# Kernel tuning notes

Hardware: AMD Instinct MI355X
Metric: run time of the kernel (lower is better)

Reference implementation:

```python
import jax, jax.numpy as jnp
import numpy as np

E = 8        # numExperts
D = 1024     # d_model
F = 4096     # expert hidden = 4*d_model
T = 8192     # total tokens (sum of expertFrequency)


def setup_inputs() -> dict:
    key = jax.random.key(0)
    k0, k1, k2, k3, k4 = jax.random.split(key, 5)
    expertOrderedInput = jax.random.normal(k0, (T, D), dtype=jnp.float32)
    # Static equal split so the split sizes are jit-compatible.
    expertFrequency = jnp.full((E,), T // E, dtype=jnp.int64)
    s1 = 1.0 / np.sqrt(D)
    s2 = 1.0 / np.sqrt(F)
    w1 = jax.random.normal(k1, (E, D, F), dtype=jnp.float32) * s1
    b1 = jnp.zeros((E, F), dtype=jnp.float32)
    w2 = jax.random.normal(k2, (E, F, D), dtype=jnp.float32) * s2
    b2 = jnp.zeros((E, D), dtype=jnp.float32)
    return {"expertOrderedInput": expertOrderedInput,
            "expertFrequency": expertFrequency,
            "w1": w1, "b1": b1, "w2": w2, "b2": b2}


def reference(expertOrderedInput, expertFrequency, w1, b1, w2, b2):
    # expertOrderedInput: [T, D], tokens pre-sorted by expert.
    # expertFrequency is equal per expert (T/E each), so the
    # split-loop-cat in the torch module is exactly a grouped GEMM.
    e = w1.shape[0]
    t = expertOrderedInput.shape[0]
    x = expertOrderedInput.reshape(e, t // e, -1)            # [E, T/E, D]
    h = jax.nn.gelu(jnp.einsum('etd,edf->etf', x, w1) + b1[:, None, :])
    y = jnp.einsum('etf,efd->etd', h, w2) + b2[:, None, :]   # [E, T/E, D]
    return y.reshape(t, -1)                                   # cat along dim 0
```

## Files before the change

kernel.cpp:

```cpp
#include <hip/hip_runtime.h>

#define E_ 8
#define D_ 1024
#define F_ 4096
#define T_ 8192

typedef unsigned short u16;
typedef short bf16x8 __attribute__((ext_vector_type(8)));
typedef float f32x4 __attribute__((ext_vector_type(4)));
typedef unsigned short u16x8 __attribute__((ext_vector_type(8)));
typedef unsigned short u16x2 __attribute__((ext_vector_type(2)));

__device__ __forceinline__ u16 f2bf(float f) {
    unsigned u = __builtin_bit_cast(unsigned, f);
    u += 0x7fffu + ((u >> 16) & 1u);
    return (u16)(u >> 16);
}

__device__ __forceinline__ float gelu_fast(float x) {
    const float a = -2.885390082f * 0.7978845608028654f;
    const float b = a * 0.044715f;
    float u = x * x;
    float p = x * __builtin_fmaf(b, u, a);
    float e = exp2f(p);
    return x * __builtin_amdgcn_rcpf(1.0f + e);
}

__device__ __forceinline__ void async16(const void* g, void* l) {
    __builtin_amdgcn_global_load_lds(
        (const __attribute__((address_space(1))) unsigned int*)g,
        (__attribute__((address_space(3))) unsigned int*)l, 16, 0, 0);
}

__global__ void cvt_x(const float* __restrict__ in, u16* __restrict__ out) {
    int i = blockIdx.x * 256 + threadIdx.x;
    const float4* in4 = (const float4*)in;
    float4 a = in4[2 * i], b = in4[2 * i + 1];
    u16x8 o;
    o[0] = f2bf(a.x); o[1] = f2bf(a.y); o[2] = f2bf(a.z); o[3] = f2bf(a.w);
    o[4] = f2bf(b.x); o[5] = f2bf(b.y); o[6] = f2bf(b.z); o[7] = f2bf(b.w);
    *(u16x8*)(out + (size_t)i * 8) = o;
}

__global__ __launch_bounds__(256) void transpose_cvt(
    const float* __restrict__ src, u16* __restrict__ dst, int R, int C) {
    __shared__ float tile[32][129];
    int e = blockIdx.z;
    src += (size_t)e * R * C;
    dst += (size_t)e * R * C;
    int c0 = blockIdx.x * 32, r0 = blockIdx.y * 128;
    int tid = threadIdx.x;
    int lc = tid & 31, lr0 = tid >> 5;
#pragma unroll
    for (int i = 0; i < 16; ++i) {
        int r = lr0 + i * 8;
        tile[lc][r] = src[(size_t)(r0 + r) * C + c0 + lc];
    }
    __syncthreads();
    int sc = tid >> 6, sr = (tid & 63) * 2;
#pragma unroll
    for (int i = 0; i < 8; ++i) {
        int c = sc + i * 4;
        u16x2 v;
        v[0] = f2bf(tile[c][sr]);
        v[1] = f2bf(tile[c][sr + 1]);
        *(u16x2*)(dst + (size_t)(c0 + c) * R + r0 + sr) = v;
    }
}

template <int BN, int WM, int WN, int EPI, int NM, int NN>
__global__ __launch_bounds__(512, 2) void gemm8p(
    const u16* __restrict__ A,
    const u16* __restrict__ Bt,
    const float* __restrict__ bias,
    void* __restrict__ Cv,
    int Mpe, int N, int K) {
    constexpr int BM  = 256;
    constexpr int LA  = 2;
    constexpr int LB  = BN / 128;
    constexpr int WTM = BM / WM;
    constexpr int MFR = WTM / 16;
    constexpr int AELEM = 4 * BM * 32;
    constexpr int VMC = 2 * (LA + LB);
    __shared__ u16 lds[AELEM + 4 * BN * 32];

    const int tid = threadIdx.x;
    const int w = tid >> 6, lane = tid & 63;
    const int lr = lane & 15, lg = lane >> 4;
    const int wm = w / WN, wn = w % WN;

    constexpr int NWG = E_ * NM * NN;
    constexpr int PER = NWG / 8;
    const int bid = blockIdx.x;
    const int logical = (bid & 7) * PER + (bid >> 3);
    const int e   = logical / (NM * NN);
    const int rem = logical % (NM * NN);
    const int bn  = rem / NM;
    const int bm  = rem % NM;

    A    += (size_t)e * Mpe * K;
    Bt   += (size_t)e * N * K;
    bias += (size_t)e * N;
    const int n0 = bn * BN;
    const int m0 = bm * BM;
    const int NT = K >> 6;

    const char* gA[LA];
    const char* gB[LB];
    {
        int kch = (lane & 3) ^ ((lane >> 3) & 3);
#pragma unroll
        for (int i = 0; i < LA; ++i) {
            int row = i * 128 + w * 16 + (lane >> 2);
            gA[i] = (const char*)(A + (size_t)(m0 + row) * K + kch * 8);
        }
#pragma unroll
        for (int i = 0; i < LB; ++i) {
            int row = i * 128 + w * 16 + (lane >> 2);
            gB[i] = (const char*)(Bt + (size_t)(n0 + row) * K + kch * 8);
        }
    }
    char* ldsc = (char*)lds;

    auto stageA = [&](int t, int h) {
        size_t goff = (size_t)t * 128 + (size_t)h * 64;
        unsigned dst = (unsigned)((((t & 1) * 2 + h) * (BM * 64)) + w * 1024);
#pragma unroll
        for (int i = 0; i < LA; ++i)
            async16(gA[i] + goff, ldsc + dst + i * 8192);
    };
    auto stageB = [&](int t, int h) {
        size_t goff = (size_t)t * 128 + (size_t)h * 64;
        unsigned dst = (unsigned)(AELEM * 2 + (((t & 1) * 2 + h) * (BN * 64)) + w * 1024);
#pragma unroll
        for (int i = 0; i < LB; ++i)
            async16(gB[i] + goff, ldsc + dst + i * 8192);
    };

    f32x4 acc[MFR][4];
    const f32x4 zero = {0.f, 0.f, 0.f, 0.f};
#pragma unroll
    for (int i = 0; i < MFR; ++i)
#pragma unroll
        for (int j = 0; j < 4; ++j) acc[i][j] = zero;

    stageA(0, 0); stageB(0, 0); stageA(0, 1); stageB(0, 1);
    stageA(1, 0); stageB(1, 0);
    asm volatile("s_waitcnt vmcnt(%0)" :: "i"(VMC) : "memory");
    __builtin_amdgcn_s_barrier();
    __builtin_amdgcn_sched_barrier(0);

    const u16* SBbase = lds + AELEM;
    bf16x8 a[MFR];
    const int arow = wm * WTM + lr;
    const int brow = wn * 64 + lr;
    const int axor = (lg ^ ((arow >> 1) & 3)) * 8;
    const int bxor = (lg ^ ((brow >> 1) & 3)) * 8;

#define PH_OPEN()                                          \
    __builtin_amdgcn_sched_barrier(0);                     \
    __builtin_amdgcn_s_barrier();                          \
    asm volatile("s_waitcnt lgkmcnt(0)" ::: "memory");     \
    __builtin_amdgcn_sched_barrier(0);                     \
    __builtin_amdgcn_s_setprio(1);
#define PH_CLOSE()                                         \
    __builtin_amdgcn_s_setprio(0);                         \
    __builtin_amdgcn_sched_barrier(0);                     \
    __builtin_amdgcn_s_barrier();                          \
    __builtin_amdgcn_sched_barrier(0);
#define PH_CLOSE_VM()                                      \
    __builtin_amdgcn_s_setprio(0);                         \
    __builtin_amdgcn_sched_barrier(0);                     \
    if (tail) asm volatile("s_waitcnt vmcnt(0)" ::: "memory");                \
    else      asm volatile("s_waitcnt vmcnt(%0)" :: "i"(VMC) : "memory");     \
    __builtin_amdgcn_s_barrier();                          \
    __builtin_amdgcn_sched_barrier(0);

#pragma unroll 2
    for (int c = 0; c < NT; ++c) {
        const int bb = c & 1;
        const u16* SA0 = lds    + (bb * 2 + 0) * (BM * 32);
        const u16* SA1 = lds    + (bb * 2 + 1) * (BM * 32);
        const u16* SB0 = SBbase + (bb * 2 + 0) * (BN * 32);
        const u16* SB1 = SBbase + (bb * 2 + 1) * (BN * 32);
        const bool stg1 = (c + 1 < NT);
        const bool stg2 = (c + 2 < NT);
        const bool tail = (c >= NT - 2);

#pragma unroll
        for (int i = 0; i < MFR; ++i)
            a[i] = *(const bf16x8*)(SA0 + (arow + i * 16) * 32 + axor);
        bf16x8 b0 = *(const bf16x8*)(SB0 + (brow +  0) * 32 + bxor);
        bf16x8 b1 = *(const bf16x8*)(SB0 + (brow + 16) * 32 + bxor);
        if (stg1) stageA(c + 1, 1);
        PH_OPEN();
#pragma unroll
        for (int i = 0; i < MFR; ++i) {
            acc[i][0] = __builtin_amdgcn_mfma_f32_16x16x32_bf16(a[i], b0, acc[i][0], 0, 0, 0);
            acc[i][1] = __builtin_amdgcn_mfma_f32_16x16x32_bf16(a[i], b1, acc[i][1], 0, 0, 0);
        }
        PH_CLOSE();

        b0 = *(const bf16x8*)(SB0 + (brow + 32) * 32 + bxor);
        b1 = *(const bf16x8*)(SB0 + (brow + 48) * 32 + bxor);
        if (stg1) stageB(c + 1, 1);
        PH_OPEN();
#pragma unroll
        for (int i = 0; i < MFR; ++i) {
            acc[i][2] = __builtin_amdgcn_mfma_f32_16x16x32_bf16(a[i], b0, acc[i][2], 0, 0, 0);
            acc[i][3] = __builtin_amdgcn_mfma_f32_16x16x32_bf16(a[i], b1, acc[i][3], 0, 0, 0);
        }
        PH_CLOSE_VM();

#pragma unroll
        for (int i = 0; i < MFR; ++i)
            a[i] = *(const bf16x8*)(SA1 + (arow + i * 16) * 32 + axor);
        b0 = *(const bf16x8*)(SB1 + (brow +  0) * 32 + bxor);
        b1 = *(const bf16x8*)(SB1 + (brow + 16) * 32 + bxor);
        if (stg2) stageA(c + 2, 0);
        PH_OPEN();
#pragma unroll
        for (int i = 0; i < MFR; ++i) {
            acc[i][0] = __builtin_amdgcn_mfma_f32_16x16x32_bf16(a[i], b0, acc[i][0], 0, 0, 0);
            acc[i][1] = __builtin_amdgcn_mfma_f32_16x16x32_bf16(a[i], b1, acc[i][1], 0, 0, 0);
        }
        PH_CLOSE();

        b0 = *(const bf16x8*)(SB1 + (brow + 32) * 32 + bxor);
        b1 = *(const bf16x8*)(SB1 + (brow + 48) * 32 + bxor);
        if (stg2) stageB(c + 2, 0);
        PH_OPEN();
#pragma unroll
        for (int i = 0; i < MFR; ++i) {
            acc[i][2] = __builtin_amdgcn_mfma_f32_16x16x32_bf16(a[i], b0, acc[i][2], 0, 0, 0);
            acc[i][3] = __builtin_amdgcn_mfma_f32_16x16x32_bf16(a[i], b1, acc[i][3], 0, 0, 0);
        }
        PH_CLOSE_VM();
    }
#undef PH_OPEN
#undef PH_CLOSE
#undef PH_CLOSE_VM

    const int mb = m0 + wm * WTM, nb = n0 + wn * 64;
    if constexpr (EPI == 1) {
        u16* C = (u16*)Cv + (size_t)e * Mpe * N;
#pragma unroll
        for (int i = 0; i < MFR; ++i) {
#pragma unroll
            for (int j = 0; j < 4; ++j) {
                int col = nb + j * 16 + lr;
                float bv = bias[col];
                int row = mb + i * 16 + lg * 4;
#pragma unroll
                for (int t = 0; t < 4; ++t) {
                    float v = acc[i][j][t] + bv;
                    C[(size_t)(row + t) * N + col] = f2bf(gelu_fast(v));
                }
            }
        }
    } else {
        float* C = (float*)Cv + (size_t)e * Mpe * N;
#pragma unroll
        for (int i = 0; i < MFR; ++i) {
#pragma unroll
            for (int j = 0; j < 4; ++j) {
                int col = nb + j * 16 + lr;
                float bv = bias[col];
                int row = mb + i * 16 + lg * 4;
#pragma unroll
                for (int t = 0; t < 4; ++t)
                    C[(size_t)(row + t) * N + col] = acc[i][j][t] + bv;
            }
        }
    }
}

extern "C" void kernel_launch(void* const* d_in, const int* in_sizes, int n_in,
                              void* d_out, int out_size, void* d_ws, size_t ws_size,
                              hipStream_t stream) {
    const float* X  = (const float*)d_in[0];
    const float* w1 = (const float*)d_in[2];
    const float* b1 = (const float*)d_in[3];
    const float* w2 = (const float*)d_in[4];
    const float* b2 = (const float*)d_in[5];
    float* out = (float*)d_out;

    const size_t XBF_B = (size_t)T_ * D_ * 2;
    const size_t WT_B  = (size_t)E_ * F_ * D_ * 2;
    const size_t H_B   = (size_t)T_ * F_ * 2;
    if (ws_size < XBF_B + WT_B + H_B) return;

    char* ws = (char*)d_ws;
    u16* Xbf = (u16*)ws;
    u16* Wt  = (u16*)(ws + XBF_B);
    u16* H   = (u16*)(ws + XBF_B + WT_B);

    cvt_x<<<dim3((T_ * D_) / 8 / 256), dim3(256), 0, stream>>>(X, Xbf);
    transpose_cvt<<<dim3(F_ / 32, D_ / 128, E_), dim3(256), 0, stream>>>(w1, Wt, D_, F_);
    gemm8p<256, 2, 4, 1, 4, 16><<<dim3(512), dim3(512), 0, stream>>>(
        Xbf, Wt, b1, H, T_ / E_, F_, D_);
    transpose_cvt<<<dim3(D_ / 32, F_ / 128, E_), dim3(256), 0, stream>>>(w2, Wt, F_, D_);
    gemm8p<128, 4, 2, 0, 4, 8><<<dim3(256), dim3(512), 0, stream>>>(
        H, Wt, b2, out, T_ / E_, D_, F_);
}
```

Measured before the change: 250.7 us.

## Restructure GEMM main loop to 4 phases with register double-buffered LDS reads

Rewrites the GEMM inner loop from 8 barrier-delimited phases into 4 phases per iteration. LDS fragment reads for the next MFMA block are issued before the current block executes, using separate a_cur/a_nxt and bA/bB register sets. The warp layout is fixed at 4x2 waves with 64-row wave tiles, and the vmcnt waits are retuned to the new staging order. This removes half of the workgroup barriers and overlaps LDS latency with MFMA work, at the cost of more live registers and more intricate wait accounting.

```diff
diff --git a/kernel.cpp b/kernel.cpp
--- a/kernel.cpp
+++ b/kernel.cpp
@@ -68,8 +68,8 @@
     }
 }
 
-template <int BN, int WM, int WN, int EPI, int NM, int NN>
-__global__ __launch_bounds__(512, 2) void gemm8p(
+template <int BN, int EPI, int NM, int NN>
+__global__ __launch_bounds__(512, 2) void gemm4p(
     const u16* __restrict__ A,
     const u16* __restrict__ Bt,
     const float* __restrict__ bias,
@@ -78,16 +78,19 @@
     constexpr int BM  = 256;
     constexpr int LA  = 2;
     constexpr int LB  = BN / 128;
-    constexpr int WTM = BM / WM;
-    constexpr int MFR = WTM / 16;
+    constexpr int MFR = 4;
+    constexpr int NFR = BN / 2 / 16;
+    constexpr int NH  = NFR / 2;
     constexpr int AELEM = 4 * BM * 32;
-    constexpr int VMC = 2 * (LA + LB);
+    constexpr int VMP = 2 * LA + LB;
+    constexpr int VMT = LA + LB;
+    constexpr int VPR = 2 * (LA + LB);
     __shared__ u16 lds[AELEM + 4 * BN * 32];
 
     const int tid = threadIdx.x;
     const int w = tid >> 6, lane = tid & 63;
     const int lr = lane & 15, lg = lane >> 4;
-    const int wm = w / WN, wn = w % WN;
+    const int wm = w >> 1, wn = w & 1;
 
     constexpr int NWG = E_ * NM * NN;
     constexpr int PER = NWG / 8;
@@ -137,42 +140,53 @@
             async16(gB[i] + goff, ldsc + dst + i * 8192);
     };
 
-    f32x4 acc[MFR][4];
+    f32x4 acc[MFR][NFR];
     const f32x4 zero = {0.f, 0.f, 0.f, 0.f};
 #pragma unroll
     for (int i = 0; i < MFR; ++i)
 #pragma unroll
-        for (int j = 0; j < 4; ++j) acc[i][j] = zero;
+        for (int j = 0; j < NFR; ++j) acc[i][j] = zero;
+
+    const u16* SBbase = lds + AELEM;
+    const int arow = wm * 64 + lr;
+    const int nbase = wn * (BN / 2) + lr;
+    const int axor = (lg ^ ((arow >> 1) & 3)) * 8;
+    const int bxor = (lg ^ ((nbase >> 1) & 3)) * 8;
+
+    bf16x8 a_cur[MFR], a_nxt[MFR], bA[NH], bB[NH];
 
     stageA(0, 0); stageB(0, 0); stageA(0, 1); stageB(0, 1);
     stageA(1, 0); stageB(1, 0);
-    asm volatile("s_waitcnt vmcnt(%0)" :: "i"(VMC) : "memory");
+    asm volatile("s_waitcnt vmcnt(%0)" :: "i"(VPR) : "memory");
     __builtin_amdgcn_s_barrier();
     __builtin_amdgcn_sched_barrier(0);
-
-    const u16* SBbase = lds + AELEM;
-    bf16x8 a[MFR];
-    const int arow = wm * WTM + lr;
-    const int brow = wn * 64 + lr;
-    const int axor = (lg ^ ((arow >> 1) & 3)) * 8;
-    const int bxor = (lg ^ ((brow >> 1) & 3)) * 8;
-
-#define PH_OPEN()                                          \
+    {
+        const u16* SA0 = lds;
+        const u16* SB0 = SBbase;
+#pragma unroll
+        for (int i = 0; i < MFR; ++i)
+            a_cur[i] = *(const bf16x8*)(SA0 + (arow + i * 16) * 32 + axor);
+#pragma unroll
+        for (int j = 0; j < NH; ++j)
+            bA[j] = *(const bf16x8*)(SB0 + (nbase + j * 16) * 32 + bxor);
+    }
+    asm volatile("s_waitcnt lgkmcnt(0)" ::: "memory");
+    __builtin_amdgcn_sched_barrier(0);
+
+#define MFMA_BLK(AARR, BARR, J0)                                              \
+    __builtin_amdgcn_s_setprio(1);                                            \
+    _Pragma("unroll")                                                         \
+    for (int i = 0; i < MFR; ++i) {                                           \
+        _Pragma("unroll")                                                     \
+        for (int j = 0; j < NH; ++j)                                          \
+            acc[i][(J0) + j] = __builtin_amdgcn_mfma_f32_16x16x32_bf16(       \
+                AARR[i], BARR[j], acc[i][(J0) + j], 0, 0, 0);                 \
+    }                                                                         \
+    __builtin_amdgcn_s_setprio(0);
+
+#define PH_END()                                           \
     __builtin_amdgcn_sched_barrier(0);                     \
-    __builtin_amdgcn_s_barrier();                          \
     asm volatile("s_waitcnt lgkmcnt(0)" ::: "memory");     \
-    __builtin_amdgcn_sched_barrier(0);                     \
-    __builtin_amdgcn_s_setprio(1);
-#define PH_CLOSE()                                         \
-    __builtin_amdgcn_s_setprio(0);                         \
-    __builtin_amdgcn_sched_barrier(0);                     \
-    __builtin_amdgcn_s_barrier();                          \
-    __builtin_amdgcn_sched_barrier(0);
-#define PH_CLOSE_VM()                                      \
-    __builtin_amdgcn_s_setprio(0);                         \
-    __builtin_amdgcn_sched_barrier(0);                     \
-    if (tail) asm volatile("s_waitcnt vmcnt(0)" ::: "memory");                \
-    else      asm volatile("s_waitcnt vmcnt(%0)" :: "i"(VMC) : "memory");     \
     __builtin_amdgcn_s_barrier();                          \
     __builtin_amdgcn_sched_barrier(0);
 
@@ -183,71 +197,72 @@
         const u16* SA1 = lds    + (bb * 2 + 1) * (BM * 32);
         const u16* SB0 = SBbase + (bb * 2 + 0) * (BN * 32);
         const u16* SB1 = SBbase + (bb * 2 + 1) * (BN * 32);
+        const u16* SA0n = lds    + (((c + 1) & 1) * 2) * (BM * 32);
+        const u16* SB0n = SBbase + (((c + 1) & 1) * 2) * (BN * 32);
         const bool stg1 = (c + 1 < NT);
         const bool stg2 = (c + 2 < NT);
-        const bool tail = (c >= NT - 2);
+
+#pragma unroll
+        for (int j = 0; j < NH; ++j)
+            bB[j] = *(const bf16x8*)(SB0 + (nbase + (NH + j) * 16) * 32 + bxor);
+        if (stg1) stageA(c + 1, 1);
+        __builtin_amdgcn_sched_barrier(0);
+        MFMA_BLK(a_cur, bA, 0);
+        __builtin_amdgcn_sched_barrier(0);
+        asm volatile("s_waitcnt lgkmcnt(0)" ::: "memory");
+        if (c == NT - 1) asm volatile("s_waitcnt vmcnt(0)" ::: "memory");
+        else             asm volatile("s_waitcnt vmcnt(%0)" :: "i"(VMP) : "memory");
+        __builtin_amdgcn_s_barrier();
+        __builtin_amdgcn_sched_barrier(0);
 
 #pragma unroll
         for (int i = 0; i < MFR; ++i)
-            a[i] = *(const bf16x8*)(SA0 + (arow + i * 16) * 32 + axor);
-        bf16x8 b0 = *(const bf16x8*)(SB0 + (brow +  0) * 32 + bxor);
-        bf16x8 b1 = *(const bf16x8*)(SB0 + (brow + 16) * 32 + bxor);
-        if (stg1) stageA(c + 1, 1);
-        PH_OPEN();
-#pragma unroll
-        for (int i = 0; i < MFR; ++i) {
-            acc[i][0] = __builtin_amdgcn_mfma_f32_16x16x32_bf16(a[i], b0, acc[i][0], 0, 0, 0);
-            acc[i][1] = __builtin_amdgcn_mfma_f32_16x16x32_bf16(a[i], b1, acc[i][1], 0, 0, 0);
-        }
-        PH_CLOSE();
-
-        b0 = *(const bf16x8*)(SB0 + (brow + 32) * 32 + bxor);
-        b1 = *(const bf16x8*)(SB0 + (brow + 48) * 32 + bxor);
+            a_nxt[i] = *(const bf16x8*)(SA1 + (arow + i * 16) * 32 + axor);
+#pragma unroll
+        for (int j = 0; j < NH; ++j)
+            bA[j] = *(const bf16x8*)(SB1 + (nbase + j * 16) * 32 + bxor);
         if (stg1) stageB(c + 1, 1);
-        PH_OPEN();
-#pragma unroll
-        for (int i = 0; i < MFR; ++i) {
-            acc[i][2] = __builtin_amdgcn_mfma_f32_16x16x32_bf16(a[i], b0, acc[i][2], 0, 0, 0);
-            acc[i][3] = __builtin_amdgcn_mfma_f32_16x16x32_bf16(a[i], b1, acc[i][3], 0, 0, 0);
-        }
-        PH_CLOSE_VM();
-
-#pragma unroll
-        for (int i = 0; i < MFR; ++i)
-            a[i] = *(const bf16x8*)(SA1 + (arow + i * 16) * 32 + axor);
-        b0 = *(const bf16x8*)(SB1 + (brow +  0) * 32 + bxor);
-        b1 = *(const bf16x8*)(SB1 + (brow + 16) * 32 + bxor);
+        __builtin_amdgcn_sched_barrier(0);
+        MFMA_BLK(a_cur, bB, NH);
+        PH_END();
+
+#pragma unroll
+        for (int j = 0; j < NH; ++j)
+            bB[j] = *(const bf16x8*)(SB1 + (nbase + (NH + j) * 16) * 32 + bxor);
         if (stg2) stageA(c + 2, 0);
-        PH_OPEN();
-#pragma unroll
-        for (int i = 0; i < MFR; ++i) {
-            acc[i][0] = __builtin_amdgcn_mfma_f32_16x16x32_bf16(a[i], b0, acc[i][0], 0, 0, 0);
-            acc[i][1] = __builtin_amdgcn_mfma_f32_16x16x32_bf16(a[i], b1, acc[i][1], 0, 0, 0);
-        }
-        PH_CLOSE();
-
-        b0 = *(const bf16x8*)(SB1 + (brow + 32) * 32 + bxor);
-        b1 = *(const bf16x8*)(SB1 + (brow + 48) * 32 + bxor);
+        __builtin_amdgcn_sched_barrier(0);
+        MFMA_BLK(a_nxt, bA, 0);
+        __builtin_amdgcn_sched_barrier(0);
+        asm volatile("s_waitcnt lgkmcnt(0)" ::: "memory");
+        if (c == NT - 1)      asm volatile("s_waitcnt vmcnt(0)" ::: "memory");
+        else if (c == NT - 2) asm volatile("s_waitcnt vmcnt(%0)" :: "i"(VMT) : "memory");
+        else                  asm volatile("s_waitcnt vmcnt(%0)" :: "i"(VMP) : "memory");
+        __builtin_amdgcn_s_barrier();
+        __builtin_amdgcn_sched_barrier(0);
+
+        if (c + 1 < NT) {
+#pragma unroll
+            for (int i = 0; i < MFR; ++i)
+                a_cur[i] = *(const bf16x8*)(SA0n + (arow + i * 16) * 32 + axor);
+#pragma unroll
+            for (int j = 0; j < NH; ++j)
+                bA[j] = *(const bf16x8*)(SB0n + (nbase + j * 16) * 32 + bxor);
+        }
         if (stg2) stageB(c + 2, 0);
-        PH_OPEN();
-#pragma unroll
-        for (int i = 0; i < MFR; ++i) {
-            acc[i][2] = __builtin_amdgcn_mfma_f32_16x16x32_bf16(a[i], b0, acc[i][2], 0, 0, 0);
-            acc[i][3] = __builtin_amdgcn_mfma_f32_16x16x32_bf16(a[i], b1, acc[i][3], 0, 0, 0);
-        }
-        PH_CLOSE_VM();
-    }
-#undef PH_OPEN
-#undef PH_CLOSE
-#undef PH_CLOSE_VM
-
-    const int mb = m0 + wm * WTM, nb = n0 + wn * 64;
+        __builtin_amdgcn_sched_barrier(0);
+        MFMA_BLK(a_nxt, bB, NH);
+        PH_END();
+    }
+#undef MFMA_BLK
+#undef PH_END
+
+    const int mb = m0 + wm * 64, nb = n0 + wn * (BN / 2);
     if constexpr (EPI == 1) {
         u16* C = (u16*)Cv + (size_t)e * Mpe * N;
 #pragma unroll
         for (int i = 0; i < MFR; ++i) {
 #pragma unroll
-            for (int j = 0; j < 4; ++j) {
+            for (int j = 0; j < NFR; ++j) {
                 int col = nb + j * 16 + lr;
                 float bv = bias[col];
                 int row = mb + i * 16 + lg * 4;
@@ -263,7 +278,7 @@
 #pragma unroll
         for (int i = 0; i < MFR; ++i) {
 #pragma unroll
-            for (int j = 0; j < 4; ++j) {
+            for (int j = 0; j < NFR; ++j) {
                 int col = nb + j * 16 + lr;
                 float bv = bias[col];
                 int row = mb + i * 16 + lg * 4;
@@ -297,9 +312,9 @@
 
     cvt_x<<<dim3((T_ * D_) / 8 / 256), dim3(256), 0, stream>>>(X, Xbf);
     transpose_cvt<<<dim3(F_ / 32, D_ / 128, E_), dim3(256), 0, stream>>>(w1, Wt, D_, F_);
-    gemm8p<256, 2, 4, 1, 4, 16><<<dim3(512), dim3(512), 0, stream>>>(
+    gemm4p<256, 1, 4, 16><<<dim3(512), dim3(512), 0, stream>>>(
         Xbf, Wt, b1, H, T_ / E_, F_, D_);
     transpose_cvt<<<dim3(D_ / 32, F_ / 128, E_), dim3(256), 0, stream>>>(w2, Wt, F_, D_);
-    gemm8p<128, 4, 2, 0, 4, 8><<<dim3(256), dim3(512), 0, stream>>>(
+    gemm4p<128, 0, 4, 8><<<dim3(256), dim3(512), 0, stream>>>(
         H, Wt, b2, out, T_ / E_, D_, F_);
 }
```

Measured after the change: 248.4 us. No clear change (-0.9%).
